# Kernel tuning notes

Hardware: AMD Instinct MI355X
Metric: run time of the kernel (lower is better)

The kernel has to match this reference:

```python
import jax, jax.numpy as jnp
import numpy as np

B, S, D = 2, 2048, 1024
H, DH, DL, DR = 16, 64, 512, 64
DHID, N_SHARED, N_ROUTED, TOPK = 512, 2, 8, 2
EPS = 1e-6


def setup_inputs() -> dict:
    key = jax.random.key(0)
    ks = jax.random.split(key, 16)
    w = lambda k, shp: jax.random.normal(k, shp, dtype=jnp.float32) * 0.02
    return {
        "x": jax.random.normal(ks[0], (B, S, D), dtype=jnp.float32),
        "mask": jnp.tril(jnp.ones((S, S), dtype=bool)),  # causal
        "w_q": w(ks[1], (D, H * (DH + DR))),
        "w_dkv": w(ks[2], (D, DL)),
        "w_uk": w(ks[3], (DL, H * DH)),
        "w_uv": w(ks[4], (DL, H * DH)),
        "w_kr": w(ks[5], (D, DR)),
        "w_o": w(ks[6], (H * DH, D)),
        "attn_norm_w": jnp.ones((D,), jnp.float32),
        "mlp_norm_w": jnp.ones((D,), jnp.float32),
        "gate_w": w(ks[7], (D, N_ROUTED)),
        "wr_gate": w(ks[8], (N_ROUTED, D, DHID)),
        "wr_up": w(ks[9], (N_ROUTED, D, DHID)),
        "wr_down": w(ks[10], (N_ROUTED, DHID, D)),
        "ws_gate": w(ks[11], (N_SHARED, D, DHID)),
        "ws_up": w(ks[12], (N_SHARED, D, DHID)),
        "ws_down": w(ks[13], (N_SHARED, DHID, D)),
    }


def _rmsnorm(x, w):
    x32 = x.astype(jnp.float32)
    n = x32 * jax.lax.rsqrt(jnp.mean(x32 * x32, axis=-1, keepdims=True) + EPS)
    return n.astype(x.dtype) * w


def _rope_tables(seq_len, dim):
    half = dim // 2
    inv = 1.0 / (10000.0 ** (jnp.arange(half, dtype=jnp.float32) / half))
    ang = jnp.arange(seq_len, dtype=jnp.float32)[:, None] * inv[None, :]  # [S, dim/2]
    return jnp.cos(ang), jnp.sin(ang)


def _rope(t, cos, sin):
    # t: [..., S, dim]; rotate-half convention
    t1, t2 = jnp.split(t, 2, axis=-1)
    return jnp.concatenate([t1 * cos - t2 * sin, t2 * cos + t1 * sin], axis=-1)


def _layer(x, mask, w_q, w_dkv, w_uk, w_uv, w_kr, w_o, attn_norm_w, mlp_norm_w,
           gate_w, wr_gate, wr_up, wr_down, ws_gate, ws_up, ws_down):
    # ---- pre-norm MLA attention + residual ----
    h = _rmsnorm(x, attn_norm_w)
    cos, sin = _rope_tables(S, DR)

    q = (h @ w_q).reshape(B, S, H, DH + DR).transpose(0, 2, 1, 3)  # [B,H,S,DH+DR]
    q_c, q_r = q[..., :DH], _rope(q[..., DH:], cos, sin)

    latent = h @ w_dkv                                              # [B,S,DL]
    k_c = (latent @ w_uk).reshape(B, S, H, DH).transpose(0, 2, 1, 3)  # [B,H,S,DH]
    v = (latent @ w_uv).reshape(B, S, H, DH).transpose(0, 2, 1, 3)
    k_r = _rope(h @ w_kr, cos, sin)                                 # [B,S,DR] shared across heads

    scale = 1.0 / np.sqrt(DH + DR)
    scores = (jnp.einsum("bhqd,bhkd->bhqk", q_c, k_c)
              + jnp.einsum("bhqd,bkd->bhqk", q_r, k_r)) * scale
    scores = jnp.where(mask, scores, jnp.float32(-1e9))
    attn = jax.nn.softmax(scores, axis=-1)
    ctx = jnp.einsum("bhqk,bhkd->bhqd", attn, v)                    # [B,H,S,DH]
    attn_out = ctx.transpose(0, 2, 1, 3).reshape(B, S, H * DH) @ w_o
    x = x + attn_out

    # ---- pre-norm shared + routed MoE FFN + residual ----
    h = _rmsnorm(x, mlp_norm_w).reshape(-1, D)                      # [T,D]
    probs = jax.nn.softmax(h @ gate_w, axis=-1)                     # [T,NR]
    vals, idx = jax.lax.top_k(probs, TOPK)                          # [T,K]
    gw = vals / jnp.sum(vals, axis=-1, keepdims=True)
    dense_w = jnp.sum(jax.nn.one_hot(idx, N_ROUTED, dtype=h.dtype) * gw[..., None], axis=1)  # [T,NR]

    g = jax.nn.silu(jnp.einsum("td,edh->teh", h, wr_gate))
    u = jnp.einsum("td,edh->teh", h, wr_up)
    y = jnp.einsum("teh,ehd->ted", g * u, wr_down)                  # [T,NR,D]
    routed = jnp.einsum("ted,te->td", y, dense_w)

    gs = jax.nn.silu(jnp.einsum("td,sdh->tsh", h, ws_gate))
    us = jnp.einsum("td,sdh->tsh", h, ws_up)
    shared = jnp.einsum("tsh,shd->td", gs * us, ws_down)

    return x + (routed + shared).reshape(B, S, D)


def reference(x, mask, w_q, w_dkv, w_uk, w_uv, w_kr, w_o, attn_norm_w, mlp_norm_w,
              gate_w, wr_gate, wr_up, wr_down, ws_gate, ws_up, ws_down):
    return _layer(x, mask, w_q, w_dkv, w_uk, w_uv, w_kr, w_o, attn_norm_w, mlp_norm_w,
                  gate_w, wr_gate, wr_up, wr_down, ws_gate, ws_up, ws_down)
```

## Files before the change

### kernel.cpp

```cpp
#include <hip/hip_runtime.h>
#include <hip/hip_bf16.h>
#include <stdint.h>

typedef unsigned short u16;
typedef __attribute__((ext_vector_type(8))) short short8;
typedef __attribute__((ext_vector_type(4))) float f32x4;
typedef __attribute__((ext_vector_type(4))) int i32x4;
typedef __attribute__((ext_vector_type(2))) unsigned int u32x2;

#define B_    2
#define S_    2048
#define D_    1024
#define H_    16
#define T_    (B_*S_)

static __device__ __forceinline__ float b2f(u16 h) { return __uint_as_float(((uint32_t)h) << 16); }
static __device__ __forceinline__ u16 f2b(float f) {
    uint32_t u = __float_as_uint(f);
    u += 0x7fffu + ((u >> 16) & 1u);
    return (u16)(u >> 16);
}
static __device__ __forceinline__ uint32_t pack2(float a, float b) {
    return (uint32_t)f2b(a) | ((uint32_t)f2b(b) << 16);
}
static __device__ __forceinline__ uint32_t cvtpk(float a, float b) {
    uint32_t r;
    asm("v_cvt_pk_bf16_f32 %0, %1, %2" : "=v"(r) : "v"(a), "v"(b));
    return r;
}
#define MFMA(a,b,c) __builtin_amdgcn_mfma_f32_16x16x32_bf16(a,b,c,0,0,0)

static __device__ __forceinline__ void gl2lds16(const void* g, void* l) {
    __builtin_amdgcn_global_load_lds((const __attribute__((address_space(1))) void*)g,
                                     (__attribute__((address_space(3))) void*)l, 16, 0, 0);
}

__global__ __launch_bounds__(256) void transpose_cvt(const float* __restrict__ in,
    u16* __restrict__ out, int K, int N, long inEZ, long outEZ)
{
    __shared__ float tile[32][33];
    const int e = blockIdx.z;
    const float* ip = in + (long)e * inEZ;
    u16* op = out + (long)e * outEZ;
    int n0 = blockIdx.x * 32, k0 = blockIdx.y * 32;
    int tx = threadIdx.x, ty = threadIdx.y;
#pragma unroll
    for (int i = 0; i < 4; ++i) {
        int k = k0 + ty + 8 * i, n = n0 + tx;
        tile[ty + 8 * i][tx] = (k < K && n < N) ? ip[(long)k * N + n] : 0.f;
    }
    __syncthreads();
#pragma unroll
    for (int i = 0; i < 4; ++i) {
        int n = n0 + ty + 8 * i, k = k0 + tx;
        if (n < N && k < K) op[(long)n * K + k] = f2b(tile[tx][ty + 8 * i]);
    }
}

__global__ __launch_bounds__(256) void gemm_k(const u16* __restrict__ A, long lda,
    const u16* __restrict__ Bt, long ldb, void* __restrict__ Cv, long ldc, int K,
    int mode, const float* __restrict__ resid)
{
    __shared__ u16 As[128 * 32];
    __shared__ u16 Bs[128 * 32];
    const int tid = threadIdx.x, lane = tid & 63, wave = tid >> 6;
    const int wm = (wave & 1) * 64, wn = (wave >> 1) * 64;
    const int quad = lane >> 4, rr = lane & 15, q8 = quad * 8;
    const long row0 = (long)blockIdx.y * 128, col0 = (long)blockIdx.x * 128;
    f32x4 acc[4][4];
#pragma unroll
    for (int i = 0; i < 4; ++i)
#pragma unroll
        for (int j = 0; j < 4; ++j)
#pragma unroll
            for (int c = 0; c < 4; ++c) acc[i][j][c] = 0.f;
    const int band = wave * 32;
    const u16* ga = A + (row0 + band + (lane >> 2)) * lda + (lane & 3) * 8;
    const u16* gb = Bt + (col0 + band + (lane >> 2)) * ldb + (lane & 3) * 8;
    u16* la = &As[band * 32];
    u16* lb = &Bs[band * 32];
    for (int k0 = 0; k0 < K; k0 += 32) {
        gl2lds16(ga + k0, la);
        gl2lds16(ga + k0 + 16 * lda, la + 16 * 32);
        gl2lds16(gb + k0, lb);
        gl2lds16(gb + k0 + 16 * ldb, lb + 16 * 32);
        __syncthreads();
        short8 af[4], bf[4];
#pragma unroll
        for (int mi = 0; mi < 4; ++mi) af[mi] = *(const short8*)&As[(wm + mi * 16 + rr) * 32 + q8];
#pragma unroll
        for (int ni = 0; ni < 4; ++ni) bf[ni] = *(const short8*)&Bs[(wn + ni * 16 + rr) * 32 + q8];
#pragma unroll
        for (int mi = 0; mi < 4; ++mi)
#pragma unroll
            for (int ni = 0; ni < 4; ++ni)
                acc[mi][ni] = MFMA(af[mi], bf[ni], acc[mi][ni]);
        __syncthreads();
    }
#pragma unroll
    for (int mi = 0; mi < 4; ++mi)
#pragma unroll
        for (int ni = 0; ni < 4; ++ni)
#pragma unroll
            for (int rg = 0; rg < 4; ++rg) {
                long r = row0 + wm + mi * 16 + quad * 4 + rg;
                long c = col0 + wn + ni * 16 + rr;
                float v = acc[mi][ni][rg];
                if (mode == 1)      ((u16*)Cv)[r * ldc + c] = f2b(v);
                else if (mode == 2) ((float*)Cv)[r * ldc + c] += v;
                else                ((float*)Cv)[r * ldc + c] = v + resid[r * 1024 + c];
            }
}

__global__ __launch_bounds__(256) void gemm_gather(const u16* __restrict__ H2,
    const u16* __restrict__ BtAll, u16* __restrict__ C,
    const int* __restrict__ cnt, const int* __restrict__ off,
    const int* __restrict__ elist)
{
    const int e = blockIdx.z;
    const int cntE = cnt[e], offE = off[e];
    const int m0 = blockIdx.y * 128;
    if (m0 >= cntE) return;
    const u16* Bt = BtAll + (long)e * 1024 * 1024;
    __shared__ u16 As[128 * 32];
    __shared__ u16 Bs[128 * 32];
    const int tid = threadIdx.x, lane = tid & 63, wave = tid >> 6;
    const int wm = (wave & 1) * 64, wn = (wave >> 1) * 64;
    const int quad = lane >> 4, rr = lane & 15, q8 = quad * 8;
    const long col0 = (long)blockIdx.x * 128;
    f32x4 acc[4][4];
#pragma unroll
    for (int i = 0; i < 4; ++i)
#pragma unroll
        for (int j = 0; j < 4; ++j)
#pragma unroll
            for (int c = 0; c < 4; ++c) acc[i][j][c] = 0.f;
    const int band = wave * 32;
    int r0 = m0 + band + (lane >> 2);
    int r1 = r0 + 16;
    int tok0 = elist[offE + (r0 < cntE ? r0 : cntE - 1)];
    int tok1 = elist[offE + (r1 < cntE ? r1 : cntE - 1)];
    const u16* ga0 = H2 + (long)tok0 * 1024 + (lane & 3) * 8;
    const u16* ga1 = H2 + (long)tok1 * 1024 + (lane & 3) * 8;
    const u16* gb = Bt + (col0 + band + (lane >> 2)) * 1024L + (lane & 3) * 8;
    u16* la = &As[band * 32];
    u16* lb = &Bs[band * 32];
    for (int k0 = 0; k0 < 1024; k0 += 32) {
        gl2lds16(ga0 + k0, la);
        gl2lds16(ga1 + k0, la + 16 * 32);
        gl2lds16(gb + k0, lb);
        gl2lds16(gb + k0 + 16 * 1024, lb + 16 * 32);
        __syncthreads();
        short8 af[4], bf[4];
#pragma unroll
        for (int mi = 0; mi < 4; ++mi) af[mi] = *(const short8*)&As[(wm + mi * 16 + rr) * 32 + q8];
#pragma unroll
        for (int ni = 0; ni < 4; ++ni) bf[ni] = *(const short8*)&Bs[(wn + ni * 16 + rr) * 32 + q8];
#pragma unroll
        for (int mi = 0; mi < 4; ++mi)
#pragma unroll
            for (int ni = 0; ni < 4; ++ni)
                acc[mi][ni] = MFMA(af[mi], bf[ni], acc[mi][ni]);
        __syncthreads();
    }
#pragma unroll
    for (int mi = 0; mi < 4; ++mi)
#pragma unroll
        for (int ni = 0; ni < 4; ++ni)
#pragma unroll
            for (int rg = 0; rg < 4; ++rg) {
                int ml = wm + mi * 16 + quad * 4 + rg;
                long c = col0 + wn + ni * 16 + rr;
                if (m0 + ml < cntE)
                    C[(long)(offE + m0 + ml) * 1024 + c] = f2b(acc[mi][ni][rg]);
            }
}

__global__ __launch_bounds__(256) void gemm_slot(const u16* __restrict__ Act,
    const u16* __restrict__ BtAll, u16* __restrict__ rout,
    const int* __restrict__ cnt, const int* __restrict__ off)
{
    const int e = blockIdx.z;
    const int cntE = cnt[e], offE = off[e];
    const int m0 = blockIdx.y * 128;
    if (m0 >= cntE) return;
    const u16* Bt = BtAll + (long)e * 1024 * 512;
    __shared__ u16 As[128 * 32];
    __shared__ u16 Bs[128 * 32];
    const int tid = threadIdx.x, lane = tid & 63, wave = tid >> 6;
    const int wm = (wave & 1) * 64, wn = (wave >> 1) * 64;
    const int quad = lane >> 4, rr = lane & 15, q8 = quad * 8;
    const long col0 = (long)blockIdx.x * 128;
    f32x4 acc[4][4];
#pragma unroll
    for (int i = 0; i < 4; ++i)
#pragma unroll
        for (int j = 0; j < 4; ++j)
#pragma unroll
            for (int c = 0; c < 4; ++c) acc[i][j][c] = 0.f;
    const int band = wave * 32;
    int r0 = offE + m0 + band + (lane >> 2); if (r0 > 8191) r0 = 8191;
    int r1 = r0 + 16; if (r1 > 8191) r1 = 8191;
    const u16* ga0 = Act + (long)r0 * 1024 + (lane & 3) * 8;
    const u16* ga1 = Act + (long)r1 * 1024 + (lane & 3) * 8;
    const u16* gb = Bt + (col0 + band + (lane >> 2)) * 512L + (lane & 3) * 8;
    u16* la = &As[band * 32];
    u16* lb = &Bs[band * 32];
    for (int k0 = 0; k0 < 512; k0 += 32) {
        gl2lds16(ga0 + k0, la);
        gl2lds16(ga1 + k0, la + 16 * 32);
        gl2lds16(gb + k0, lb);
        gl2lds16(gb + k0 + 16 * 512, lb + 16 * 32);
        __syncthreads();
        short8 af[4], bf[4];
#pragma unroll
        for (int mi = 0; mi < 4; ++mi) af[mi] = *(const short8*)&As[(wm + mi * 16 + rr) * 32 + q8];
#pragma unroll
        for (int ni = 0; ni < 4; ++ni) bf[ni] = *(const short8*)&Bs[(wn + ni * 16 + rr) * 32 + q8];
#pragma unroll
        for (int mi = 0; mi < 4; ++mi)
#pragma unroll
            for (int ni = 0; ni < 4; ++ni)
                acc[mi][ni] = MFMA(af[mi], bf[ni], acc[mi][ni]);
        __syncthreads();
    }
#pragma unroll
    for (int mi = 0; mi < 4; ++mi)
#pragma unroll
        for (int ni = 0; ni < 4; ++ni)
#pragma unroll
            for (int rg = 0; rg < 4; ++rg) {
                int ml = wm + mi * 16 + quad * 4 + rg;
                long c = col0 + wn + ni * 16 + rr;
                if (m0 + ml < cntE)
                    rout[(long)(offE + m0 + ml) * 1024 + c] = f2b(acc[mi][ni][rg]);
            }
}

__global__ __launch_bounds__(256) void rmsnorm_wave(const float* __restrict__ x,
    const float* __restrict__ w, u16* __restrict__ out)
{
    const int t = blockIdx.x * 4 + (threadIdx.x >> 6);
    const int lane = threadIdx.x & 63;
    const float* xp = x + (size_t)t * D_;
    f32x4 v[4];
    float s = 0.f;
#pragma unroll
    for (int i = 0; i < 4; ++i) {
        v[i] = *(const f32x4*)&xp[lane * 4 + i * 256];
#pragma unroll
        for (int j = 0; j < 4; ++j) s += v[i][j] * v[i][j];
    }
#pragma unroll
    for (int o = 32; o > 0; o >>= 1) s += __shfl_xor(s, o);
    const float inv = rsqrtf(s * (1.f / D_) + 1e-6f);
    u16* op = out + (size_t)t * D_;
#pragma unroll
    for (int i = 0; i < 4; ++i) {
        const int d = lane * 4 + i * 256;
        f32x4 wv = *(const f32x4*)&w[d];
        u32x2 pk;
        pk[0] = pack2(v[i][0] * inv * wv[0], v[i][1] * inv * wv[1]);
        pk[1] = pack2(v[i][2] * inv * wv[2], v[i][3] * inv * wv[3]);
        *(u32x2*)&op[d] = pk;
    }
}

__global__ __launch_bounds__(256) void rmsnorm_gate_fused(const float* __restrict__ xm,
    const float* __restrict__ nw, const float* __restrict__ gw, u16* __restrict__ h2,
    int* __restrict__ tok_e, float* __restrict__ tok_w)
{
    const int t = blockIdx.x * 4 + (threadIdx.x >> 6);
    const int lane = threadIdx.x & 63;
    const float* xp = xm + (size_t)t * D_;
    f32x4 v[4];
    float s = 0.f;
#pragma unroll
    for (int i = 0; i < 4; ++i) {
        v[i] = *(const f32x4*)&xp[lane * 4 + i * 256];
#pragma unroll
        for (int j = 0; j < 4; ++j) s += v[i][j] * v[i][j];
    }
#pragma unroll
    for (int o = 32; o > 0; o >>= 1) s += __shfl_xor(s, o);
    const float inv = rsqrtf(s * (1.f / D_) + 1e-6f);
    u16* op = h2 + (size_t)t * D_;
    float part[8] = {0,0,0,0,0,0,0,0};
#pragma unroll
    for (int i = 0; i < 4; ++i) {
        const int d = lane * 4 + i * 256;
        f32x4 wv = *(const f32x4*)&nw[d];
        float hv[4];
#pragma unroll
        for (int j = 0; j < 4; ++j) hv[j] = v[i][j] * inv * wv[j];
        u32x2 pk;
        pk[0] = pack2(hv[0], hv[1]);
        pk[1] = pack2(hv[2], hv[3]);
        *(u32x2*)&op[d] = pk;
#pragma unroll
        for (int j = 0; j < 4; ++j) {
            const float* gp = gw + (size_t)(d + j) * 8;
#pragma unroll
            for (int e = 0; e < 8; ++e) part[e] += hv[j] * gp[e];
        }
    }
#pragma unroll
    for (int e = 0; e < 8; ++e)
#pragma unroll
        for (int o = 32; o > 0; o >>= 1) part[e] += __shfl_xor(part[e], o);
    if (lane == 0) {
        float mx = part[0];
#pragma unroll
        for (int e = 1; e < 8; ++e) mx = fmaxf(mx, part[e]);
        float p[8];
#pragma unroll
        for (int e = 0; e < 8; ++e) p[e] = __expf(part[e] - mx);
        int i0 = 0;
#pragma unroll
        for (int e = 1; e < 8; ++e) if (p[e] > p[i0]) i0 = e;
        int i1 = (i0 == 0) ? 1 : 0;
#pragma unroll
        for (int e = 0; e < 8; ++e) { if (e == i0) continue; if (p[e] > p[i1]) i1 = e; }
        float sw = p[i0] + p[i1];
        tok_e[2 * t] = i0;  tok_e[2 * t + 1] = i1;
        tok_w[2 * t] = p[i0] / sw;  tok_w[2 * t + 1] = p[i1] / sw;
    }
}

__global__ __launch_bounds__(256) void moe_route(const int* __restrict__ tok_e,
    int* __restrict__ cnt, int* __restrict__ off,
    int* __restrict__ elist, int* __restrict__ tslot)
{
    const int E = blockIdx.x;
    const int tid = threadIdx.x, lane = tid & 63, wave = tid >> 6;
    int ev[32];
#pragma unroll
    for (int i = 0; i < 8; ++i)
        *(i32x4*)&ev[i * 4] = *(const i32x4*)&tok_e[tid * 32 + i * 4];
    int c8[8] = {0,0,0,0,0,0,0,0};
#pragma unroll
    for (int k = 0; k < 32; ++k) ++c8[ev[k] & 7];
    int incl[8];
#pragma unroll
    for (int e = 0; e < 8; ++e) {
        int vv = c8[e];
#pragma unroll
        for (int d = 1; d < 64; d <<= 1) {
            int tmp = __shfl_up(vv, d);
            if (lane >= d) vv += tmp;
        }
        incl[e] = vv;
    }
    __shared__ int wtot[4][8];
    if (lane == 63)
#pragma unroll
        for (int e = 0; e < 8; ++e) wtot[wave][e] = incl[e];
    __syncthreads();
    int tot[8];
#pragma unroll
    for (int e = 0; e < 8; ++e) tot[e] = wtot[0][e] + wtot[1][e] + wtot[2][e] + wtot[3][e];
    int waveoff = 0;
    for (int w = 0; w < 4; ++w) if (w < wave) waveoff += wtot[w][E];
    int offE = 0;
#pragma unroll
    for (int e = 0; e < 8; ++e) if (e < E) offE += tot[e];
    int rank = offE + waveoff + (incl[E] - c8[E]);
#pragma unroll
    for (int k = 0; k < 32; ++k) {
        if ((ev[k] & 7) == E) {
            int p = tid * 32 + k;
            elist[rank] = p >> 1;
            tslot[p] = rank;
            ++rank;
        }
    }
    if (tid == 0) { cnt[E] = tot[E]; off[E] = offE; }
}

__global__ __launch_bounds__(256) void rope_q_kernel(u16* __restrict__ proj)
{
    int idx = blockIdx.x * 256 + threadIdx.x;
    int i  = idx & 31;
    int hh = (idx >> 5) & (H_ - 1);
    int t  = idx >> 9;
    int s  = t & (S_ - 1);
    float inv = __expf(-(float)i * 0.28782313662425575f);
    float ang = (float)s * inv;
    float c = cosf(ang), sn = sinf(ang);
    u16* base = proj + (size_t)t * 2688 + hh * 128 + 64;
    float t1 = b2f(base[i]), t2 = b2f(base[32 + i]);
    base[i]      = f2b(t1 * c - t2 * sn);
    base[32 + i] = f2b(t2 * c + t1 * sn);
}

__global__ __launch_bounds__(256) void rope_kr_kernel(u16* __restrict__ proj)
{
    int idx = blockIdx.x * 256 + threadIdx.x;
    int i = idx & 31;
    int t = idx >> 5;
    int s = t & (S_ - 1);
    float inv = __expf(-(float)i * 0.28782313662425575f);
    float ang = (float)s * inv;
    float c = cosf(ang), sn = sinf(ang);
    u16* base = proj + (size_t)t * 2688 + 2560;
    float t1 = b2f(base[i]), t2 = b2f(base[32 + i]);
    base[i]      = f2b(t1 * c - t2 * sn);
    base[32 + i] = f2b(t2 * c + t1 * sn);
}

#define KS  136
#define PS2 72
__global__ __launch_bounds__(256) void attn_flash(const u16* __restrict__ proj,
    const u16* __restrict__ kc, const u16* __restrict__ vt, u16* __restrict__ ctx)
{
    const int qidx = blockIdx.x >> 5;
    const int qt = (qidx < 16) ? (31 - qidx) : (qidx - 16);
    const int bh = blockIdx.x & 31;
    const int b = bh >> 4, h = bh & 15;
    const int q0 = qt * 64;
    const int tid = threadIdx.x, lane = tid & 63, wave = tid >> 6;
    const int quad = lane >> 4, rr = lane & 15, q8 = quad * 8;
    const int wm2 = wave * 16;

    __shared__ u16 Ks[64 * KS];
    __shared__ u16 Ps[64 * PS2];

    const long tbase = (long)b * S_ + q0;
    short8 qf[4];
#pragma unroll
    for (int d0 = 0; d0 < 4; ++d0)
        qf[d0] = *(const short8*)&proj[(tbase + wm2 + rr) * 2688 + h * 128 + d0 * 32 + q8];

    f32x4 accO[4];
    float m_i = -3e38f, l_i = 0.f;
#pragma unroll
    for (int vi = 0; vi < 4; ++vi)
#pragma unroll
        for (int rg = 0; rg < 4; ++rg) accO[vi][rg] = 0.f;
    const float sc = 0.08838834764831845f * 1.4426950408889634f;

    const u16* vbase = vt + (size_t)(h * 64 + rr) * 4096 + b * 2048 + q8;

    const int nkt = qt + 1;
    for (int kt = 0; kt < nkt; ++kt) {
        const int k0 = kt * 64;
        const long kb = (long)b * S_ + k0;
#pragma unroll
        for (int i = 0; i < 2; ++i) {
            int c = tid + i * 256, row = c >> 3, cc = (c & 7) * 8;
            *(short8*)&Ks[row * KS + cc] = *(const short8*)&kc[(kb + row) * 1024 + h * 64 + cc];
        }
#pragma unroll
        for (int i = 0; i < 2; ++i) {
            int c = tid + i * 256, row = c >> 3, cc = (c & 7) * 8;
            *(short8*)&Ks[row * KS + 64 + cc] = *(const short8*)&proj[(kb + row) * 2688 + 2560 + cc];
        }
        __syncthreads();

        f32x4 accS[4];
#pragma unroll
        for (int ki = 0; ki < 4; ++ki)
#pragma unroll
            for (int rg = 0; rg < 4; ++rg) accS[ki][rg] = 0.f;
#pragma unroll
        for (int d0 = 0; d0 < 4; ++d0) {
            short8 kf[4];
#pragma unroll
            for (int ki = 0; ki < 4; ++ki) kf[ki] = *(const short8*)&Ks[(ki * 16 + rr) * KS + d0 * 32 + q8];
#pragma unroll
            for (int ki = 0; ki < 4; ++ki) accS[ki] = MFMA(kf[ki], qf[d0], accS[ki]);
        }
        __syncthreads();

        short8 vf0[4], vf1[4];
#pragma unroll
        for (int vi = 0; vi < 4; ++vi) {
            vf0[vi] = *(const short8*)(vbase + (size_t)vi * 16 * 4096 + k0);
            vf1[vi] = *(const short8*)(vbase + (size_t)vi * 16 * 4096 + k0 + 32);
        }

        float mx = -3e38f;
        if (kt == qt) {
            const int qg = q0 + wm2 + rr;
#pragma unroll
            for (int ki = 0; ki < 4; ++ki)
#pragma unroll
                for (int rg = 0; rg < 4; ++rg) {
                    float w = accS[ki][rg] * sc;
                    if (k0 + ki * 16 + quad * 4 + rg > qg) w = -1e30f;
                    accS[ki][rg] = w;
                    mx = fmaxf(mx, w);
                }
        } else {
#pragma unroll
            for (int ki = 0; ki < 4; ++ki)
#pragma unroll
                for (int rg = 0; rg < 4; ++rg) {
                    float w = accS[ki][rg] * sc;
                    accS[ki][rg] = w;
                    mx = fmaxf(mx, w);
                }
        }
        mx = fmaxf(mx, __shfl_xor(mx, 16));
        mx = fmaxf(mx, __shfl_xor(mx, 32));
        if (__any(mx > m_i)) {
            float mnew = fmaxf(m_i, mx);
            float alpha = exp2f(m_i - mnew);
            m_i = mnew;
            l_i *= alpha;
#pragma unroll
            for (int vi = 0; vi < 4; ++vi)
#pragma unroll
                for (int rg = 0; rg < 4; ++rg) accO[vi][rg] *= alpha;
        }
        float ps = 0.f;
#pragma unroll
        for (int ki = 0; ki < 4; ++ki) {
            float p0 = exp2f(accS[ki][0] - m_i);
            float p1 = exp2f(accS[ki][1] - m_i);
            float p2 = exp2f(accS[ki][2] - m_i);
            float p3 = exp2f(accS[ki][3] - m_i);
            ps += (p0 + p1) + (p2 + p3);
            u32x2 pk; pk[0] = cvtpk(p0, p1); pk[1] = cvtpk(p2, p3);
            *(u32x2*)&Ps[(wm2 + rr) * PS2 + ki * 16 + quad * 4] = pk;
        }
        ps += __shfl_xor(ps, 16);
        ps += __shfl_xor(ps, 32);
        l_i += ps;

        short8 pf0 = *(const short8*)&Ps[(wm2 + rr) * PS2 + q8];
        short8 pf1 = *(const short8*)&Ps[(wm2 + rr) * PS2 + 32 + q8];
#pragma unroll
        for (int vi = 0; vi < 4; ++vi) accO[vi] = MFMA(vf0[vi], pf0, accO[vi]);
#pragma unroll
        for (int vi = 0; vi < 4; ++vi) accO[vi] = MFMA(vf1[vi], pf1, accO[vi]);
    }
    {
        float linv = 1.f / l_i;
        long t = tbase + wm2 + rr;
#pragma unroll
        for (int vi = 0; vi < 4; ++vi) {
            u32x2 pk;
            pk[0] = pack2(accO[vi][0] * linv, accO[vi][1] * linv);
            pk[1] = pack2(accO[vi][2] * linv, accO[vi][3] * linv);
            *(u32x2*)&ctx[t * 1024 + h * 64 + vi * 16 + quad * 4] = pk;
        }
    }
}

__global__ __launch_bounds__(256) void silu_mul(u16* __restrict__ gu, int nPairRows)
{
    int i = blockIdx.x * 256 + threadIdx.x;
    if (i >= nPairRows * 64) return;
    int row = i >> 6, j8 = (i & 63) * 8;
    long base = (long)row * 1024;
    short8 g8 = *(const short8*)&gu[base + j8];
    short8 u8 = *(const short8*)&gu[base + 512 + j8];
    short8 r;
#pragma unroll
    for (int j = 0; j < 8; ++j) {
        float g = b2f((u16)g8[j]), u = b2f((u16)u8[j]);
        r[j] = (short)f2b(g / (1.f + __expf(-g)) * u);
    }
    *(short8*)&gu[base + j8] = r;
}

__global__ __launch_bounds__(256) void final_kernel(const float* __restrict__ xm,
    const u16* __restrict__ rout, const int* __restrict__ tok_slot,
    const float* __restrict__ tok_w, float* __restrict__ out)
{
    long i = ((long)blockIdx.x * 256 + threadIdx.x) * 4;
    int t = (int)(i >> 10), d = (int)(i & 1023);
    int s0 = tok_slot[2 * t], s1 = tok_slot[2 * t + 1];
    float w0 = tok_w[2 * t], w1 = tok_w[2 * t + 1];
    f32x4 xv = *(const f32x4*)&xm[i];
    u32x2 r0 = *(const u32x2*)&rout[(long)s0 * 1024 + d];
    u32x2 r1 = *(const u32x2*)&rout[(long)s1 * 1024 + d];
    f32x4 o;
    o[0] = xv[0] + w0 * b2f((u16)(r0[0] & 0xffffu)) + w1 * b2f((u16)(r1[0] & 0xffffu));
    o[1] = xv[1] + w0 * b2f((u16)(r0[0] >> 16))     + w1 * b2f((u16)(r1[0] >> 16));
    o[2] = xv[2] + w0 * b2f((u16)(r0[1] & 0xffffu)) + w1 * b2f((u16)(r1[1] & 0xffffu));
    o[3] = xv[3] + w0 * b2f((u16)(r0[1] >> 16))     + w1 * b2f((u16)(r1[1] >> 16));
    *(f32x4*)&out[i] = o;
}

#define OFF_XMID   0UL
#define OFF_H      16777216UL
#define OFF_PROJ   25165824UL
#define OFF_WGU    25165824UL
#define OFF_KC     47185920UL
#define OFF_WD     47185920UL
#define OFF_VT     55574528UL
#define OFF_GUR    57671680UL
#define OFF_CTX    63963136UL
#define OFF_WATT   72351744UL
#define OFF_ROUT   74448896UL
#define OFF_GUS    91226112UL
#define OFF_TOKE   108003328UL
#define OFF_TOKW   108036096UL
#define OFF_TSLOT  108068864UL
#define OFF_ELIST  108101632UL
#define OFF_META   108134400UL

extern "C" void kernel_launch(void* const* d_in, const int* in_sizes, int n_in,
                              void* d_out, int out_size, void* d_ws, size_t ws_size,
                              hipStream_t stream)
{
    const float* x       = (const float*)d_in[0];
    const float* w_q     = (const float*)d_in[2];
    const float* w_dkv   = (const float*)d_in[3];
    const float* w_uk    = (const float*)d_in[4];
    const float* w_uv    = (const float*)d_in[5];
    const float* w_kr    = (const float*)d_in[6];
    const float* w_o     = (const float*)d_in[7];
    const float* attn_nw = (const float*)d_in[8];
    const float* mlp_nw  = (const float*)d_in[9];
    const float* gate_w  = (const float*)d_in[10];
    const float* wr_gate = (const float*)d_in[11];
    const float* wr_up   = (const float*)d_in[12];
    const float* wr_down = (const float*)d_in[13];
    const float* ws_gate = (const float*)d_in[14];
    const float* ws_up   = (const float*)d_in[15];
    const float* ws_down = (const float*)d_in[16];
    float* out = (float*)d_out;

    char* W = (char*)d_ws;
    float* x_mid = (float*)(W + OFF_XMID);
    u16* h      = (u16*)(W + OFF_H);
    u16* h2     = (u16*)(W + OFF_H);
    u16* proj   = (u16*)(W + OFF_PROJ);
    u16* wgu_t  = (u16*)(W + OFF_WGU);
    u16* kc     = (u16*)(W + OFF_KC);
    u16* wd_t   = (u16*)(W + OFF_WD);
    u16* vt     = (u16*)(W + OFF_VT);
    u16* gu_r   = (u16*)(W + OFF_GUR);
    u16* ctx    = (u16*)(W + OFF_CTX);
    u16* wqkv_t = (u16*)(W + OFF_WATT);
    u16* wuk_t  = wqkv_t + 2688 * 1024;
    u16* wuv_t  = wuk_t + 1024 * 512;
    u16* wo_t   = wuv_t + 1024 * 512;
    u16* rout   = (u16*)(W + OFF_ROUT);
    u16* gu_s   = (u16*)(W + OFF_GUS);
    int*   tok_e = (int*)(W + OFF_TOKE);
    float* tok_w = (float*)(W + OFF_TOKW);
    int*   tslot = (int*)(W + OFF_TSLOT);
    int*   elist = (int*)(W + OFF_ELIST);
    int*   meta  = (int*)(W + OFF_META);
    int* cnt = meta, * off = meta + 8;

    dim3 tb(32, 8);
    transpose_cvt<<<dim3(64, 32, 1), tb, 0, stream>>>(w_q,   wqkv_t,               1024, 2048, 0, 0);
    transpose_cvt<<<dim3(16, 32, 1), tb, 0, stream>>>(w_dkv, wqkv_t + 2048 * 1024, 1024, 512,  0, 0);
    transpose_cvt<<<dim3(2,  32, 1), tb, 0, stream>>>(w_kr,  wqkv_t + 2560 * 1024, 1024, 64,   0, 0);
    transpose_cvt<<<dim3(32, 16, 1), tb, 0, stream>>>(w_uk,  wuk_t,                512,  1024, 0, 0);
    transpose_cvt<<<dim3(32, 16, 1), tb, 0, stream>>>(w_uv,  wuv_t,                512,  1024, 0, 0);
    transpose_cvt<<<dim3(32, 32, 1), tb, 0, stream>>>(w_o,   wo_t,                 1024, 1024, 0, 0);

    rmsnorm_wave<<<T_ / 4, 256, 0, stream>>>(x, attn_nw, h);
    gemm_k<<<dim3(21, 32), 256, 0, stream>>>(h, 1024, wqkv_t, 1024, proj, 2688, 1024, 1, nullptr);
    rope_q_kernel<<<(T_ * H_ * 32) / 256, 256, 0, stream>>>(proj);
    rope_kr_kernel<<<(T_ * 32) / 256, 256, 0, stream>>>(proj);
    gemm_k<<<dim3(8, 32), 256, 0, stream>>>(proj + 2048, 2688, wuk_t, 512, kc, 1024, 512, 1, nullptr);
    gemm_k<<<dim3(32, 8), 256, 0, stream>>>(wuv_t, 512, proj + 2048, 2688, vt, 4096, 512, 1, nullptr);
    attn_flash<<<1024, 256, 0, stream>>>(proj, kc, vt, ctx);
    gemm_k<<<dim3(8, 32), 256, 0, stream>>>(ctx, 1024, wo_t, 1024, x_mid, 1024, 1024, 3, x);

    transpose_cvt<<<dim3(16, 32, 8), tb, 0, stream>>>(wr_gate, wgu_t,              1024, 512, 524288, 1048576);
    transpose_cvt<<<dim3(16, 32, 8), tb, 0, stream>>>(wr_up,   wgu_t + 512 * 1024, 1024, 512, 524288, 1048576);
    transpose_cvt<<<dim3(16, 32, 2), tb, 0, stream>>>(ws_gate, wgu_t + 8 * 1048576,              1024, 512, 524288, 1048576);
    transpose_cvt<<<dim3(16, 32, 2), tb, 0, stream>>>(ws_up,   wgu_t + 8 * 1048576 + 512 * 1024, 1024, 512, 524288, 1048576);
    transpose_cvt<<<dim3(32, 16, 8), tb, 0, stream>>>(wr_down, wd_t,               512, 1024, 524288, 524288);
    transpose_cvt<<<dim3(32, 16, 2), tb, 0, stream>>>(ws_down, wd_t + 8 * 524288,  512, 1024, 524288, 524288);

    rmsnorm_gate_fused<<<T_ / 4, 256, 0, stream>>>(x_mid, mlp_nw, gate_w, h2, tok_e, tok_w);
    moe_route<<<8, 256, 0, stream>>>(tok_e, cnt, off, elist, tslot);
    gemm_gather<<<dim3(8, 64, 8), 256, 0, stream>>>(h2, wgu_t, gu_r, cnt, off, elist);
    silu_mul<<<(8192 * 64) / 256, 256, 0, stream>>>(gu_r, 8192);
    gemm_slot<<<dim3(8, 64, 8), 256, 0, stream>>>(gu_r, wd_t, rout, cnt, off);
    gemm_k<<<dim3(16, 32), 256, 0, stream>>>(h2, 1024, wgu_t + 8 * 1048576, 1024, gu_s, 2048, 1024, 1, nullptr);
    silu_mul<<<(8192 * 64) / 256, 256, 0, stream>>>(gu_s, 8192);
    gemm_k<<<dim3(8, 32), 256, 0, stream>>>(gu_s, 2048, wd_t + 8 * 524288, 512, x_mid, 1024, 512, 2, nullptr);
    gemm_k<<<dim3(8, 32), 256, 0, stream>>>(gu_s + 1024, 2048, wd_t + 9 * 524288, 512, x_mid, 1024, 512, 2, nullptr);
    final_kernel<<<(T_ * D_) / 1024, 256, 0, stream>>>(x_mid, rout, tslot, tok_w, out);
}
```

Measured before the change: 622.5 us.

## Fuse rope kernels, merge shared-down GEMMs, load attention K directly from global

Combines the q and k_r rope kernels into one launch. Merges the two shared-expert down-projection GEMMs into a single kernel that runs K=1024 across both experts, which removes one read-modify-write pass over x_mid. In flash attention, K fragments are read straight from global memory rather than staged through LDS, which drops two barriers per tile, and a min-blocks-per-CU launch bound is added for occupancy. The risk is that uncoalesced global K reads could cost more than the removed LDS traffic.

Result: slower. 674.5 us (+8.4%).

```diff
diff --git a/kernel.cpp b/kernel.cpp
--- a/kernel.cpp
+++ b/kernel.cpp
@@ -109,6 +109,61 @@
                 if (mode == 1)      ((u16*)Cv)[r * ldc + c] = f2b(v);
                 else if (mode == 2) ((float*)Cv)[r * ldc + c] += v;
                 else                ((float*)Cv)[r * ldc + c] = v + resid[r * 1024 + c];
+            }
+}
+
+__global__ __launch_bounds__(256) void gemm_shdown(const u16* __restrict__ A,
+    const u16* __restrict__ BtBase, float* __restrict__ Cv)
+{
+    __shared__ u16 As[128 * 32];
+    __shared__ u16 Bs[128 * 32];
+    const int tid = threadIdx.x, lane = tid & 63, wave = tid >> 6;
+    const int wm = (wave & 1) * 64, wn = (wave >> 1) * 64;
+    const int quad = lane >> 4, rr = lane & 15, q8 = quad * 8;
+    const long row0 = (long)blockIdx.y * 128, col0 = (long)blockIdx.x * 128;
+    f32x4 acc[4][4];
+#pragma unroll
+    for (int i = 0; i < 4; ++i)
+#pragma unroll
+        for (int j = 0; j < 4; ++j)
+#pragma unroll
+            for (int c = 0; c < 4; ++c) acc[i][j][c] = 0.f;
+    const int band = wave * 32;
+    const long arow = row0 + band + (lane >> 2);
+    const long brow = col0 + band + (lane >> 2);
+    u16* la = &As[band * 32];
+    u16* lb = &Bs[band * 32];
+    for (int k0 = 0; k0 < 1024; k0 += 32) {
+        const long aoff = (k0 < 512) ? (long)k0 : (long)(512 + k0);
+        const long boff = (k0 < 512) ? (long)k0 : (long)(524288 - 512 + k0);
+        const u16* ga = A + arow * 2048 + aoff + (lane & 3) * 8;
+        const u16* gb = BtBase + brow * 512 + boff + (lane & 3) * 8;
+        gl2lds16(ga, la);
+        gl2lds16(ga + 16 * 2048, la + 16 * 32);
+        gl2lds16(gb, lb);
+        gl2lds16(gb + 16 * 512, lb + 16 * 32);
+        __syncthreads();
+        short8 af[4], bf[4];
+#pragma unroll
+        for (int mi = 0; mi < 4; ++mi) af[mi] = *(const short8*)&As[(wm + mi * 16 + rr) * 32 + q8];
+#pragma unroll
+        for (int ni = 0; ni < 4; ++ni) bf[ni] = *(const short8*)&Bs[(wn + ni * 16 + rr) * 32 + q8];
+#pragma unroll
+        for (int mi = 0; mi < 4; ++mi)
+#pragma unroll
+            for (int ni = 0; ni < 4; ++ni)
+                acc[mi][ni] = MFMA(af[mi], bf[ni], acc[mi][ni]);
+        __syncthreads();
+    }
+#pragma unroll
+    for (int mi = 0; mi < 4; ++mi)
+#pragma unroll
+        for (int ni = 0; ni < 4; ++ni)
+#pragma unroll
+            for (int rg = 0; rg < 4; ++rg) {
+                long r = row0 + wm + mi * 16 + quad * 4 + rg;
+                long c = col0 + wn + ni * 16 + rr;
+                Cv[r * 1024 + c] += acc[mi][ni][rg];
             }
 }
 
@@ -377,40 +432,24 @@
     if (tid == 0) { cnt[E] = tot[E]; off[E] = offE; }
 }
 
-__global__ __launch_bounds__(256) void rope_q_kernel(u16* __restrict__ proj)
-{
-    int idx = blockIdx.x * 256 + threadIdx.x;
-    int i  = idx & 31;
-    int hh = (idx >> 5) & (H_ - 1);
-    int t  = idx >> 9;
-    int s  = t & (S_ - 1);
-    float inv = __expf(-(float)i * 0.28782313662425575f);
-    float ang = (float)s * inv;
-    float c = cosf(ang), sn = sinf(ang);
-    u16* base = proj + (size_t)t * 2688 + hh * 128 + 64;
-    float t1 = b2f(base[i]), t2 = b2f(base[32 + i]);
-    base[i]      = f2b(t1 * c - t2 * sn);
-    base[32 + i] = f2b(t2 * c + t1 * sn);
-}
-
-__global__ __launch_bounds__(256) void rope_kr_kernel(u16* __restrict__ proj)
+__global__ __launch_bounds__(256) void rope_all(u16* __restrict__ proj)
 {
     int idx = blockIdx.x * 256 + threadIdx.x;
     int i = idx & 31;
-    int t = idx >> 5;
+    int r = idx >> 5;
+    int t = r / 17, which = r - t * 17;
     int s = t & (S_ - 1);
     float inv = __expf(-(float)i * 0.28782313662425575f);
     float ang = (float)s * inv;
     float c = cosf(ang), sn = sinf(ang);
-    u16* base = proj + (size_t)t * 2688 + 2560;
+    u16* base = proj + (size_t)t * 2688 + (which < 16 ? which * 128 + 64 : 2560);
     float t1 = b2f(base[i]), t2 = b2f(base[32 + i]);
     base[i]      = f2b(t1 * c - t2 * sn);
     base[32 + i] = f2b(t2 * c + t1 * sn);
 }
 
-#define KS  136
 #define PS2 72
-__global__ __launch_bounds__(256) void attn_flash(const u16* __restrict__ proj,
+__global__ __launch_bounds__(256, 4) void attn_flash(const u16* __restrict__ proj,
     const u16* __restrict__ kc, const u16* __restrict__ vt, u16* __restrict__ ctx)
 {
     const int qidx = blockIdx.x >> 5;
@@ -422,7 +461,6 @@
     const int quad = lane >> 4, rr = lane & 15, q8 = quad * 8;
     const int wm2 = wave * 16;
 
-    __shared__ u16 Ks[64 * KS];
     __shared__ u16 Ps[64 * PS2];
 
     const long tbase = (long)b * S_ + q0;
@@ -439,23 +477,13 @@
         for (int rg = 0; rg < 4; ++rg) accO[vi][rg] = 0.f;
     const float sc = 0.08838834764831845f * 1.4426950408889634f;
 
+    const u16* kcl = kc   + ((long)b * S_ + rr) * 1024 + h * 64 + q8;
+    const u16* krl = proj + ((long)b * S_ + rr) * 2688 + 2560 + q8;
     const u16* vbase = vt + (size_t)(h * 64 + rr) * 4096 + b * 2048 + q8;
 
     const int nkt = qt + 1;
     for (int kt = 0; kt < nkt; ++kt) {
         const int k0 = kt * 64;
-        const long kb = (long)b * S_ + k0;
-#pragma unroll
-        for (int i = 0; i < 2; ++i) {
-            int c = tid + i * 256, row = c >> 3, cc = (c & 7) * 8;
-            *(short8*)&Ks[row * KS + cc] = *(const short8*)&kc[(kb + row) * 1024 + h * 64 + cc];
-        }
-#pragma unroll
-        for (int i = 0; i < 2; ++i) {
-            int c = tid + i * 256, row = c >> 3, cc = (c & 7) * 8;
-            *(short8*)&Ks[row * KS + 64 + cc] = *(const short8*)&proj[(kb + row) * 2688 + 2560 + cc];
-        }
-        __syncthreads();
 
         f32x4 accS[4];
 #pragma unroll
@@ -464,13 +492,15 @@
             for (int rg = 0; rg < 4; ++rg) accS[ki][rg] = 0.f;
 #pragma unroll
         for (int d0 = 0; d0 < 4; ++d0) {
+            const u16* base = (d0 < 2) ? (kcl + (size_t)k0 * 1024 + d0 * 32)
+                                       : (krl + (size_t)k0 * 2688 + (d0 - 2) * 32);
+            const size_t rstep = (d0 < 2) ? (size_t)16 * 1024 : (size_t)16 * 2688;
             short8 kf[4];
 #pragma unroll
-            for (int ki = 0; ki < 4; ++ki) kf[ki] = *(const short8*)&Ks[(ki * 16 + rr) * KS + d0 * 32 + q8];
+            for (int ki = 0; ki < 4; ++ki) kf[ki] = *(const short8*)(base + ki * rstep);
 #pragma unroll
             for (int ki = 0; ki < 4; ++ki) accS[ki] = MFMA(kf[ki], qf[d0], accS[ki]);
         }
-        __syncthreads();
 
         short8 vf0[4], vf1[4];
 #pragma unroll
@@ -658,8 +688,7 @@
 
     rmsnorm_wave<<<T_ / 4, 256, 0, stream>>>(x, attn_nw, h);
     gemm_k<<<dim3(21, 32), 256, 0, stream>>>(h, 1024, wqkv_t, 1024, proj, 2688, 1024, 1, nullptr);
-    rope_q_kernel<<<(T_ * H_ * 32) / 256, 256, 0, stream>>>(proj);
-    rope_kr_kernel<<<(T_ * 32) / 256, 256, 0, stream>>>(proj);
+    rope_all<<<(T_ * 17 * 32) / 256, 256, 0, stream>>>(proj);
     gemm_k<<<dim3(8, 32), 256, 0, stream>>>(proj + 2048, 2688, wuk_t, 512, kc, 1024, 512, 1, nullptr);
     gemm_k<<<dim3(32, 8), 256, 0, stream>>>(wuv_t, 512, proj + 2048, 2688, vt, 4096, 512, 1, nullptr);
     attn_flash<<<1024, 256, 0, stream>>>(proj, kc, vt, ctx);
@@ -679,7 +708,6 @@
     gemm_slot<<<dim3(8, 64, 8), 256, 0, stream>>>(gu_r, wd_t, rout, cnt, off);
     gemm_k<<<dim3(16, 32), 256, 0, stream>>>(h2, 1024, wgu_t + 8 * 1048576, 1024, gu_s, 2048, 1024, 1, nullptr);
     silu_mul<<<(8192 * 64) / 256, 256, 0, stream>>>(gu_s, 8192);
-    gemm_k<<<dim3(8, 32), 256, 0, stream>>>(gu_s, 2048, wd_t + 8 * 524288, 512, x_mid, 1024, 512, 2, nullptr);
-    gemm_k<<<dim3(8, 32), 256, 0, stream>>>(gu_s + 1024, 2048, wd_t + 9 * 524288, 512, x_mid, 1024, 512, 2, nullptr);
+    gemm_shdown<<<dim3(8, 32), 256, 0, stream>>>(gu_s, wd_t + 8 * 524288, x_mid);
     final_kernel<<<(T_ * D_) / 1024, 256, 0, stream>>>(x_mid, rout, tslot, tok_w, out);
 }
```
